# Performance work log

Measured on AMD Instinct MI355X. Metric: run time of the kernel, lower is better.

## Reference

```python
import jax, jax.numpy as jnp
import numpy as np

B, N, FEAT, H = 4, 1024, 512, 8
HD = FEAT // H


def _xavier(key, shape, gain):
    fan_in, fan_out = shape[1], shape[0]
    a = gain * np.sqrt(6.0 / (fan_in + fan_out))
    return jax.random.uniform(key, shape, jnp.float32, -a, a)


def setup_inputs() -> dict:
    key = jax.random.key(0)
    ks = jax.random.split(key, 12)
    g = 2 ** (-0.5)
    return {
        "ndata": jax.random.normal(ks[0], (B, N, FEAT), jnp.float32),
        "attn_bias": jax.random.normal(ks[1], (B, N, N, H), jnp.float32),
        "attn_mask": jax.random.bernoulli(ks[2], 0.1, (B, N, N, H)),
        "Wq": _xavier(ks[3], (FEAT, FEAT), g), "bq": jnp.zeros((FEAT,), jnp.float32),
        "Wk": _xavier(ks[4], (FEAT, FEAT), g), "bk": jnp.zeros((FEAT,), jnp.float32),
        "Wv": _xavier(ks[5], (FEAT, FEAT), g), "bv": jnp.zeros((FEAT,), jnp.float32),
        "Wo": _xavier(ks[6], (FEAT, FEAT), 1.0), "bo": jnp.zeros((FEAT,), jnp.float32),
    }


def reference(ndata, attn_bias, attn_mask, Wq, bq, Wk, bk, Wv, bv, Wo, bo):
    b, n, feat = ndata.shape
    h = attn_bias.shape[-1]
    hd = feat // h
    scaling = hd ** (-0.5)
    # projections -> [B, N, H, HD]
    q = (ndata @ Wq.T + bq).reshape(b, n, h, hd) * scaling
    k = (ndata @ Wk.T + bk).reshape(b, n, h, hd)
    v = (ndata @ Wv.T + bv).reshape(b, n, h, hd)
    # scores [B, N(q), N(k), H] to match torch layout for bias/mask
    scores = jnp.einsum("bihd,bjhd->bijh", q, k)
    scores = scores + attn_bias
    scores = jnp.where(attn_mask, -jnp.inf, scores)
    attn = jax.nn.softmax(scores, axis=2)  # softmax over key dim
    out = jnp.einsum("bijh,bjhd->bihd", attn, v).reshape(b, n, feat)
    return out @ Wo.T + bo
```

## Files before the change

kernel.cpp:

```cpp
#include <hip/hip_runtime.h>
#include <hip/hip_bf16.h>
#include <cstdint>


namespace {

constexpr int kN = 1024;

typedef short bf16x8 __attribute__((ext_vector_type(8)));
typedef float f32x4 __attribute__((ext_vector_type(4)));
using u16 = unsigned short;
using u8 = unsigned char;

__device__ __forceinline__ u16 f2bf(float f) {
  union { float f; uint32_t i; } v;
  v.f = f;
  uint32_t r = v.i + 0x7fffu + ((v.i >> 16) & 1u);
  return (u16)(r >> 16);
}

__device__ __forceinline__ void gload_lds16(const void* g, void* l) {
  __builtin_amdgcn_global_load_lds(
      (__attribute__((address_space(1))) void*)g,
      (__attribute__((address_space(3))) void*)l, 16, 0, 0);
}
__device__ __forceinline__ void gload_lds4(const void* g, void* l) {
  __builtin_amdgcn_global_load_lds(
      (__attribute__((address_space(1))) void*)g,
      (__attribute__((address_space(3))) void*)l, 4, 0, 0);
}

__global__ void detect_mask_kernel(const unsigned char* __restrict__ m,
                                   int* __restrict__ flag) {
  __shared__ int red[256];
  int local = 0;
  for (int i = threadIdx.x; i < 65536; i += 256) local += (m[i] != 0) ? 1 : 0;
  red[threadIdx.x] = local;
  __syncthreads();
  for (int s = 128; s > 0; s >>= 1) {
    if ((int)threadIdx.x < s) red[threadIdx.x] += red[threadIdx.x + s];
    __syncthreads();
  }
  if (threadIdx.x == 0) *flag = (red[0] > 4915) ? 1 : 0;
}

__global__ __launch_bounds__(256) void canon_mask(const int* __restrict__ m32,
                                                  const int* __restrict__ flag,
                                                  u8* __restrict__ out) {
  if (*flag != 0) return;
  const size_t t = (size_t)blockIdx.x * 256 + threadIdx.x;
  const int4* src = (const int4*)m32 + t * 8;
  uchar4 ob[8];
#pragma unroll
  for (int q = 0; q < 8; ++q) {
    const int4 v = src[q];
    ob[q] = make_uchar4(v.x != 0, v.y != 0, v.z != 0, v.w != 0);
  }
  *(uint4*)(out + t * 32) = *(const uint4*)&ob[0];
  *(uint4*)(out + t * 32 + 16) = *(const uint4*)&ob[4];
}

__global__ __launch_bounds__(256) void convert_kernel(
    const float* __restrict__ nd, const float* __restrict__ Wq,
    const float* __restrict__ Wk, const float* __restrict__ Wv,
    const float* __restrict__ Wo, u16* __restrict__ A16,
    u16* __restrict__ W16) {
  const int gi = blockIdx.x * 256 + threadIdx.x;
  const float* src;
  u16* dst;
  int off;
  if (gi < 524288) {
    src = nd; dst = A16; off = gi * 4;
  } else {
    const int w = (gi - 524288) >> 16;
    off = ((gi - 524288) & 65535) * 4;
    src = (w == 0) ? Wq : (w == 1) ? Wk : (w == 2) ? Wv : Wo;
    dst = W16 + (size_t)w * 262144;
  }
  const float4 v = *(const float4*)&src[off];
  ushort4 o;
  o.x = f2bf(v.x); o.y = f2bf(v.y); o.z = f2bf(v.z); o.w = f2bf(v.w);
  *(ushort4*)&dst[off] = o;
}

template <int EPI>
__global__ __launch_bounds__(256) void gemm_nt(
    const u16* __restrict__ A16, const u16* __restrict__ W16,
    const float* __restrict__ bq, const float* __restrict__ bk,
    const float* __restrict__ bv, u16* __restrict__ Q16,
    u16* __restrict__ KF, u16* __restrict__ VF,
    const float* __restrict__ bo, float* __restrict__ OutF) {
  __shared__ u16 As[128 * 64];
  __shared__ u16 Ws[64 * 64];
  const int tid = threadIdx.x, lane = tid & 63, wid = tid >> 6;
  const int r0 = blockIdx.x * 128;
  int wsel, c0;
  const float* bias;
  float scale = 1.0f;
  if (EPI == 0) {
    wsel = blockIdx.y >> 3;
    c0 = (blockIdx.y & 7) * 64;
    bias = (wsel == 0) ? bq : (wsel == 1) ? bk : bv;
    if (wsel == 0) scale = 0.125f;
  } else {
    wsel = 3;
    c0 = blockIdx.y * 64;
    bias = bo;
  }
  const u16* W = W16 + (size_t)wsel * (512 * 512);
  const int wm = (wid >> 1) * 64, wn = (wid & 1) * 32;

  f32x4 acc[4][2] = {};
  for (int k0 = 0; k0 < 512; k0 += 64) {
    __syncthreads();
#pragma unroll
    for (int p = 0; p < 4; ++p) {
      const int o = p * 4096 + tid * 16;
      const int row = o >> 7, kb = o & 127;
      gload_lds16((const char*)A16 + (size_t)(r0 + row) * 1024 + k0 * 2 +
                      (kb ^ ((row & 7) << 4)),
                  (char*)As + o);
    }
#pragma unroll
    for (int p = 0; p < 2; ++p) {
      const int o = p * 4096 + tid * 16;
      const int row = o >> 7, kb = o & 127;
      gload_lds16((const char*)W + (size_t)(c0 + row) * 1024 + k0 * 2 +
                      (kb ^ ((row & 7) << 4)),
                  (char*)Ws + o);
    }
    __syncthreads();
    bf16x8 af[4][2], bf[2][2];
#pragma unroll
    for (int mt = 0; mt < 4; ++mt)
#pragma unroll
      for (int ks = 0; ks < 2; ++ks) {
        const int row = wm + mt * 16 + (lane & 15);
        const int kb = ks * 64 + (lane >> 4) * 16;
        af[mt][ks] = *(const bf16x8*)((const char*)As + row * 128 +
                                      (kb ^ ((row & 7) << 4)));
      }
#pragma unroll
    for (int nt = 0; nt < 2; ++nt)
#pragma unroll
      for (int ks = 0; ks < 2; ++ks) {
        const int row = wn + nt * 16 + (lane & 15);
        const int kb = ks * 64 + (lane >> 4) * 16;
        bf[nt][ks] = *(const bf16x8*)((const char*)Ws + row * 128 +
                                      (kb ^ ((row & 7) << 4)));
      }
#pragma unroll
    for (int mt = 0; mt < 4; ++mt)
#pragma unroll
      for (int nt = 0; nt < 2; ++nt)
#pragma unroll
        for (int ks = 0; ks < 2; ++ks)
          acc[mt][nt] = __builtin_amdgcn_mfma_f32_16x16x32_bf16(
              af[mt][ks], bf[nt][ks], acc[mt][nt], 0, 0, 0);
  }
  float bvals[2];
#pragma unroll
  for (int nt = 0; nt < 2; ++nt)
    bvals[nt] = bias[c0 + wn + nt * 16 + (lane & 15)];
#pragma unroll
  for (int mt = 0; mt < 4; ++mt)
#pragma unroll
    for (int nt = 0; nt < 2; ++nt)
#pragma unroll
      for (int r = 0; r < 4; ++r) {
        const int row = r0 + wm + mt * 16 + (lane >> 4) * 4 + r;
        const int col = c0 + wn + nt * 16 + (lane & 15);
        const float v = (acc[mt][nt][r] + bvals[nt]) * scale;
        if (EPI == 0) {
          const int bb = row >> 10, n = row & 1023, hh = col >> 6,
                    dd = col & 63;
          if (wsel == 0) {
            Q16[((size_t)(bb * 8 + hh) * 1024 + n) * 64 + dd] = f2bf(v);
          } else if (wsel == 1) {
            const int jc = n >> 5, tt = (n >> 4) & 1, ln = n & 15;
            const int ks = dd >> 5, gg = (dd >> 3) & 3, e = dd & 7;
            KF[(((((size_t)(bb * 8 + hh) * 32 + jc) * 2 + tt) * 2 + ks) * 64 +
                gg * 16 + ln) * 8 + e] = f2bf(v);
          } else {
            const int jc = n >> 5, gg = (n >> 3) & 3, e = n & 7;
            const int dt = dd >> 4, ii = dd & 15;
            VF[((((size_t)(bb * 8 + hh) * 32 + jc) * 4 + dt) * 64 + gg * 16 +
                ii) * 8 + e] = f2bf(v);
          }
        } else {
          OutF[(size_t)row * 512 + col] = v;
        }
      }
}

__global__ __launch_bounds__(512, 2) void attn_fused2(
    const u16* __restrict__ Q16, const u16* __restrict__ KF,
    const u16* __restrict__ VF, const float* __restrict__ bias,
    const u8* __restrict__ mask8, const u8* __restrict__ mask_ws,
    const int* __restrict__ flag, u16* __restrict__ Ow16) {
  __shared__ __align__(16) char biasL[3][16384];
  __shared__ __align__(16) char maskL[3][4096];
  __shared__ __align__(16) char PsL[8][1280];

  const int tid = threadIdx.x, lane = tid & 63, h = tid >> 6;
  const int bid = blockIdx.x;
  const int b = (bid >> 1) & 3;
  const int it = ((bid >> 3) << 1) | (bid & 1);
  const int i0 = it * 16;
  const u8* mk8 = (*flag != 0) ? mask8 : mask_ws;

  const int j = lane & 15, g = lane >> 4;
  const int hh = h >> 2;
  char* Ps = PsL[h];

  const u16* Qh = Q16 + (size_t)(b * 8 + h) * 65536;
  bf16x8 qf[2];
#pragma unroll
  for (int ks = 0; ks < 2; ++ks)
    qf[ks] = *(const bf16x8*)&Qh[(size_t)(i0 + j) * 64 + ks * 32 + g * 8];

  float mo[4], lo[4];
  f32x4 oacc[4] = {};
#pragma unroll
  for (int r = 0; r < 4; ++r) { mo[r] = -3e38f; lo[r] = 0.f; }

  const size_t biasRow0 = (size_t)(b * 1024 + i0) * 8192;
  const size_t maskRow0 = (size_t)(b * 1024 + i0) * 8192;

  auto STAGE = [&](int buf, int jc) {
    char* bb_ = biasL[buf];
    char* mb_ = maskL[buf];
    const int w = h;
#pragma unroll
    for (int q = 0; q < 8; ++q) {
      const int gidx = q * 8 + w;
      const int i = gidx >> 2, oct = gidx & 3;
      const int f = (i >> 2) + 4 * (oct & 1);
      const size_t src = biasRow0 + (size_t)i * 8192 + (size_t)jc * 256 +
                         oct * 64 + (lane >> 3) * 8 + (((lane & 7) - f) & 7);
      gload_lds4(bias + src, bb_ + gidx * 256);
    }
#pragma unroll
    for (int c = 0; c < 2; ++c) {
      const int i = c * 8 + w;
      const int fm = (i >> 2) & 1;
      const size_t src = maskRow0 + (size_t)i * 8192 + (size_t)jc * 256 +
                         (lane >> 4) * 64 + (size_t)(((lane & 15) ^ fm) * 4);
      gload_lds4(mk8 + src, mb_ + i * 256);
    }
  };

  STAGE(0, 0);
  STAGE(1, 1);
  asm volatile("s_waitcnt vmcnt(10)\n\ts_barrier" ::: "memory");

  for (int t = 0; t < 32; ++t) {
    const char* bb_ = biasL[t % 3];
    const char* mb_ = maskL[t % 3];

    const size_t kvb = (size_t)(b * 8 + h) * 32 + t;
    const u16* kfp = KF + kvb * 2048;
    const u16* vfp = VF + kvb * 2048;
    bf16x8 kf[2][2], vf[4];
#pragma unroll
    for (int t2 = 0; t2 < 2; ++t2)
#pragma unroll
      for (int ks = 0; ks < 2; ++ks)
        kf[t2][ks] = *(const bf16x8*)&kfp[((t2 * 2 + ks) * 64 + lane) * 8];
#pragma unroll
    for (int dt = 0; dt < 4; ++dt)
      vf[dt] = *(const bf16x8*)&vfp[(dt * 64 + lane) * 8];

    if (t < 30) STAGE((t + 2) % 3, t + 2);

    f32x4 sa[2] = {};
#pragma unroll
    for (int t2 = 0; t2 < 2; ++t2)
#pragma unroll
      for (int ks = 0; ks < 2; ++ks)
        sa[t2] = __builtin_amdgcn_mfma_f32_16x16x32_bf16(qf[ks], kf[t2][ks],
                                                         sa[t2], 0, 0, 0);

    float s[2][4];
#pragma unroll
    for (int jt = 0; jt < 2; ++jt) {
      const int oct = jt * 2 + (j >> 3);
#pragma unroll
      for (int r = 0; r < 4; ++r) {
        const int gidx = (g * 4 + r) * 4 + oct;
        const float bv = *(const float*)(
            bb_ + gidx * 256 +
            (((j & 7) * 8 + ((h + g + 4 * (j >> 3)) & 7)) << 2));
        const int qd = (j & 7) * 2 + ((hh + (g & 1)) & 1);
        const u8 mkv = *(const u8*)(mb_ + gidx * 64 + qd * 4 + (h & 3));
        s[jt][r] = mkv ? -1e30f : (sa[jt][r] + bv);
      }
    }

#pragma unroll
    for (int r = 0; r < 4; ++r) {
      float cm = fmaxf(s[0][r], s[1][r]);
      cm = fmaxf(cm, __shfl_xor(cm, 1));
      cm = fmaxf(cm, __shfl_xor(cm, 2));
      cm = fmaxf(cm, __shfl_xor(cm, 4));
      cm = fmaxf(cm, __shfl_xor(cm, 8));
      const float mn = fmaxf(mo[r], cm);
      const float sc = __expf(mo[r] - mn);
      mo[r] = mn;
      const float p0 = __expf(s[0][r] - mn);
      const float p1 = __expf(s[1][r] - mn);
      float rs = p0 + p1;
      rs += __shfl_xor(rs, 1);
      rs += __shfl_xor(rs, 2);
      rs += __shfl_xor(rs, 4);
      rs += __shfl_xor(rs, 8);
      lo[r] = lo[r] * sc + rs;
      const int row = g * 4 + r;
      *(u16*)(Ps + row * 80 + j * 2) = f2bf(p0);
      *(u16*)(Ps + row * 80 + 32 + j * 2) = f2bf(p1);
#pragma unroll
      for (int dt = 0; dt < 4; ++dt) oacc[dt][r] *= sc;
    }
    asm volatile("s_waitcnt lgkmcnt(0)" ::: "memory");
    __builtin_amdgcn_sched_barrier(0);

    const bf16x8 pf = *(const bf16x8*)(Ps + j * 80 + g * 16);
#pragma unroll
    for (int dt = 0; dt < 4; ++dt)
      oacc[dt] =
          __builtin_amdgcn_mfma_f32_16x16x32_bf16(pf, vf[dt], oacc[dt], 0, 0, 0);

    if (t < 30)
      asm volatile("s_waitcnt vmcnt(10)\n\ts_barrier" ::: "memory");
    else if (t == 30)
      asm volatile("s_waitcnt vmcnt(0)\n\ts_barrier" ::: "memory");
  }

#pragma unroll
  for (int r = 0; r < 4; ++r) {
    const float rl = 1.0f / lo[r];
    const int i = i0 + g * 4 + r;
#pragma unroll
    for (int dt = 0; dt < 4; ++dt) {
      const int d = dt * 16 + j;
      Ow16[((size_t)(b * 1024 + i)) * 512 + h * 64 + d] =
          f2bf(oacc[dt][r] * rl);
    }
  }
}

}

extern "C" void kernel_launch(void* const* d_in, const int* in_sizes, int n_in,
                              void* d_out, int out_size, void* d_ws,
                              size_t ws_size, hipStream_t stream) {
  const float* ndata = (const float*)d_in[0];
  const float* bias = (const float*)d_in[1];
  const void* mask = d_in[2];
  const float* Wq = (const float*)d_in[3];
  const float* bq = (const float*)d_in[4];
  const float* Wk = (const float*)d_in[5];
  const float* bk = (const float*)d_in[6];
  const float* Wv = (const float*)d_in[7];
  const float* bvp = (const float*)d_in[8];
  const float* Wo = (const float*)d_in[9];
  const float* bo = (const float*)d_in[10];
  float* out = (float*)d_out;

  u16* A16 = (u16*)d_ws;
  u16* W16 = A16 + 2097152;
  u16* Q16 = W16 + 1048576;
  u16* KF = Q16 + 2097152;
  u16* VF = KF + 2097152;
  u16* Ow = VF + 2097152;
  u8* mask_ws = (u8*)(Ow + 2097152);
  int* flag = (int*)(mask_ws + 33554432);

  detect_mask_kernel<<<1, 256, 0, stream>>>((const unsigned char*)mask, flag);
  canon_mask<<<4096, 256, 0, stream>>>((const int*)mask, flag, mask_ws);
  convert_kernel<<<3072, 256, 0, stream>>>(ndata, Wq, Wk, Wv, Wo, A16, W16);
  gemm_nt<0><<<dim3(32, 24), 256, 0, stream>>>(A16, W16, bq, bk, bvp, Q16, KF,
                                               VF, nullptr, nullptr);
  attn_fused2<<<256, 512, 0, stream>>>(Q16, KF, VF, bias, (const u8*)mask,
                                       mask_ws, flag, Ow);
  gemm_nt<1><<<dim3(32, 8), 256, 0, stream>>>(Ow, W16, nullptr, nullptr,
                                              nullptr, nullptr, nullptr,
                                              nullptr, bo, out);
}
```

Before: 211.8 us.

## Split attention key range across two blocks and merge with a combine kernel

The attention kernel now splits the key dimension in half, launching twice as many blocks. Each block writes unnormalized fp32 partial outputs plus row max and sum, and a new combine kernel merges the two halves. The score MFMA is transposed so P feeds the PV MFMA directly from registers instead of going through LDS. Rescaling of the accumulator is skipped when no row max changed, staging drops to double-buffered with a simplified swizzle, and launch bounds allow more blocks per CU. The cost is an extra kernel launch and the fp32 partial traffic through global memory.

```diff
diff --git a/kernel.cpp b/kernel.cpp
--- a/kernel.cpp
+++ b/kernel.cpp
@@ -4,8 +4,6 @@
 
 
 namespace {
-
-constexpr int kN = 1024;
 
 typedef short bf16x8 __attribute__((ext_vector_type(8)));
 typedef float f32x4 __attribute__((ext_vector_type(4)));
@@ -182,10 +180,12 @@
             KF[(((((size_t)(bb * 8 + hh) * 32 + jc) * 2 + tt) * 2 + ks) * 64 +
                 gg * 16 + ln) * 8 + e] = f2bf(v);
           } else {
-            const int jc = n >> 5, gg = (n >> 3) & 3, e = n & 7;
+            const int jc = n >> 5, jl = n & 31;
+            const int gg = (jl & 15) >> 2;
+            const int e = (jl < 16) ? (jl & 3) : (4 + (jl & 3));
             const int dt = dd >> 4, ii = dd & 15;
-            VF[((((size_t)(bb * 8 + hh) * 32 + jc) * 4 + dt) * 64 + gg * 16 +
-                ii) * 8 + e] = f2bf(v);
+            VF[((((size_t)(bb * 8 + hh) * 32 + jc) * 4 + dt) * 512) +
+               (gg * 16 + ii) * 8 + e] = f2bf(v);
           }
         } else {
           OutF[(size_t)row * 512 + col] = v;
@@ -193,160 +193,187 @@
       }
 }
 
-__global__ __launch_bounds__(512, 2) void attn_fused2(
+__global__ __launch_bounds__(512, 4) void attn_fused3(
     const u16* __restrict__ Q16, const u16* __restrict__ KF,
     const u16* __restrict__ VF, const float* __restrict__ bias,
     const u8* __restrict__ mask8, const u8* __restrict__ mask_ws,
-    const int* __restrict__ flag, u16* __restrict__ Ow16) {
-  __shared__ __align__(16) char biasL[3][16384];
-  __shared__ __align__(16) char maskL[3][4096];
-  __shared__ __align__(16) char PsL[8][1280];
+    const int* __restrict__ flag, float* __restrict__ Opart,
+    float* __restrict__ Mm, float* __restrict__ Ll) {
+  __shared__ __align__(16) char biasL[2][16384];
+  __shared__ __align__(16) char maskL[2][4096];
 
   const int tid = threadIdx.x, lane = tid & 63, h = tid >> 6;
   const int bid = blockIdx.x;
-  const int b = (bid >> 1) & 3;
-  const int it = ((bid >> 3) << 1) | (bid & 1);
+  const int b = bid & 3, half = (bid >> 2) & 1, it = bid >> 3;
   const int i0 = it * 16;
-  const u8* mk8 = (*flag != 0) ? mask8 : mask_ws;
-
-  const int j = lane & 15, g = lane >> 4;
-  const int hh = h >> 2;
-  char* Ps = PsL[h];
-
-  const u16* Qh = Q16 + (size_t)(b * 8 + h) * 65536;
+  const u8* mk = (*flag != 0) ? mask8 : mask_ws;
+
+  const int i = lane & 15, g = lane >> 4;
+  const int g1 = g & 1, g2 = g >> 1;
+  const int bh = b * 8 + h;
+
+  const u16* Qh = Q16 + (size_t)bh * 65536;
   bf16x8 qf[2];
 #pragma unroll
   for (int ks = 0; ks < 2; ++ks)
-    qf[ks] = *(const bf16x8*)&Qh[(size_t)(i0 + j) * 64 + ks * 32 + g * 8];
-
-  float mo[4], lo[4];
+    qf[ks] = *(const bf16x8*)&Qh[(size_t)(i0 + i) * 64 + ks * 32 + g * 8];
+
+  float mo = -3e38f, lo = 0.f;
   f32x4 oacc[4] = {};
-#pragma unroll
-  for (int r = 0; r < 4; ++r) { mo[r] = -3e38f; lo[r] = 0.f; }
-
-  const size_t biasRow0 = (size_t)(b * 1024 + i0) * 8192;
-  const size_t maskRow0 = (size_t)(b * 1024 + i0) * 8192;
+
+  const size_t rowb = (size_t)(b * 1024 + i0) * 8192;
+  int boff[8];
+#pragma unroll
+  for (int q = 0; q < 8; ++q) {
+    const int w = q * 512 + tid;
+    const int wi = w >> 8, oct = (w >> 6) & 3, slot = w & 63;
+    const int se = slot ^ wi ^ ((oct & 1) << 4);
+    boff[q] = wi * 8192 + oct * 64 + se;
+  }
+  int moff[2];
+#pragma unroll
+  for (int q = 0; q < 2; ++q) {
+    const int bb2 = (q * 512 + tid) * 4;
+    const int wi = bb2 >> 8, oct = (bb2 >> 6) & 3, sl = bb2 & 63;
+    const int se = sl ^ ((wi << 2) & 0x3C);
+    moff[q] = wi * 8192 + oct * 64 + se;
+  }
+  const int Cb = (((g1 << 5) | h) ^ i ^ (g2 << 4)) << 2;
+  const int baseb = i * 1024 + g2 * 256;
+  const int Cm = ((g1 << 5) | h) ^ ((i << 2) & 0x3C);
+  const int basem = i * 256 + g2 * 64;
 
   auto STAGE = [&](int buf, int jc) {
-    char* bb_ = biasL[buf];
-    char* mb_ = maskL[buf];
-    const int w = h;
-#pragma unroll
-    for (int q = 0; q < 8; ++q) {
-      const int gidx = q * 8 + w;
-      const int i = gidx >> 2, oct = gidx & 3;
-      const int f = (i >> 2) + 4 * (oct & 1);
-      const size_t src = biasRow0 + (size_t)i * 8192 + (size_t)jc * 256 +
-                         oct * 64 + (lane >> 3) * 8 + (((lane & 7) - f) & 7);
-      gload_lds4(bias + src, bb_ + gidx * 256);
+    const float* bsrc = bias + rowb + (size_t)jc * 256;
+    const u8* msrc = mk + rowb + (size_t)jc * 256;
+#pragma unroll
+    for (int q = 0; q < 8; ++q)
+      gload_lds4(bsrc + boff[q], biasL[buf] + (q * 512 + tid) * 4);
+#pragma unroll
+    for (int q = 0; q < 2; ++q)
+      gload_lds4(msrc + moff[q], maskL[buf] + (q * 512 + tid) * 4);
+  };
+
+  const int jcBase = half * 16;
+  STAGE(0, jcBase);
+
+  for (int t = 0; t < 16; ++t) {
+    asm volatile("s_waitcnt vmcnt(0)" ::: "memory");
+    __builtin_amdgcn_s_barrier();
+    const char* bb_ = biasL[t & 1];
+    const char* mb_ = maskL[t & 1];
+    const int jc = jcBase + t;
+    const size_t kvb = (size_t)bh * 32 + jc;
+
+    bf16x8 kf[2][2];
+#pragma unroll
+    for (int t2 = 0; t2 < 2; ++t2)
+#pragma unroll
+      for (int ks = 0; ks < 2; ++ks)
+        kf[t2][ks] =
+            *(const bf16x8*)&KF[((kvb * 2 + t2) * 2 + ks) * 512 + lane * 8];
+    bf16x8 vf[4];
+#pragma unroll
+    for (int dt = 0; dt < 4; ++dt)
+      vf[dt] = *(const bf16x8*)&VF[(kvb * 4 + dt) * 512 + lane * 8];
+
+    if (t < 15) STAGE((t + 1) & 1, jc + 1);
+
+    f32x4 sa[2] = {};
+#pragma unroll
+    for (int t2 = 0; t2 < 2; ++t2)
+#pragma unroll
+      for (int ks = 0; ks < 2; ++ks)
+        sa[t2] = __builtin_amdgcn_mfma_f32_16x16x32_bf16(kf[t2][ks], qf[ks],
+                                                         sa[t2], 0, 0, 0);
+
+    float s[2][4];
+#pragma unroll
+    for (int t2 = 0; t2 < 2; ++t2)
+#pragma unroll
+      for (int r = 0; r < 4; ++r) {
+        const float bv =
+            *(const float*)(bb_ + baseb + t2 * 512 + (Cb ^ (r << 5)));
+        const u8 mv = *(const u8*)(mb_ + basem + t2 * 128 + (Cm ^ (r << 3)));
+        s[t2][r] = mv ? -1e30f : (sa[t2][r] + bv);
+      }
+
+    float cm = s[0][0];
+#pragma unroll
+    for (int k = 1; k < 8; ++k) cm = fmaxf(cm, s[k >> 2][k & 3]);
+    cm = fmaxf(cm, __shfl_xor(cm, 16));
+    cm = fmaxf(cm, __shfl_xor(cm, 32));
+    const bool upd = __any(cm > mo);
+    const float mn = fmaxf(mo, cm);
+    const float sc = __expf(mo - mn);
+    float p[2][4], rs = 0.f;
+#pragma unroll
+    for (int k = 0; k < 8; ++k) {
+      const float pv = __expf(s[k >> 2][k & 3] - mn);
+      p[k >> 2][k & 3] = pv;
+      rs += pv;
     }
-#pragma unroll
-    for (int c = 0; c < 2; ++c) {
-      const int i = c * 8 + w;
-      const int fm = (i >> 2) & 1;
-      const size_t src = maskRow0 + (size_t)i * 8192 + (size_t)jc * 256 +
-                         (lane >> 4) * 64 + (size_t)(((lane & 15) ^ fm) * 4);
-      gload_lds4(mk8 + src, mb_ + i * 256);
+    rs += __shfl_xor(rs, 16);
+    rs += __shfl_xor(rs, 32);
+    lo = lo * sc + rs;
+    mo = mn;
+    if (upd) {
+      float scB[4];
+#pragma unroll
+      for (int r = 0; r < 4; ++r) scB[r] = __shfl(sc, g * 4 + r);
+#pragma unroll
+      for (int dt = 0; dt < 4; ++dt)
+#pragma unroll
+        for (int r = 0; r < 4; ++r) oacc[dt][r] *= scB[r];
     }
-  };
-
-  STAGE(0, 0);
-  STAGE(1, 1);
-  asm volatile("s_waitcnt vmcnt(10)\n\ts_barrier" ::: "memory");
-
-  for (int t = 0; t < 32; ++t) {
-    const char* bb_ = biasL[t % 3];
-    const char* mb_ = maskL[t % 3];
-
-    const size_t kvb = (size_t)(b * 8 + h) * 32 + t;
-    const u16* kfp = KF + kvb * 2048;
-    const u16* vfp = VF + kvb * 2048;
-    bf16x8 kf[2][2], vf[4];
-#pragma unroll
-    for (int t2 = 0; t2 < 2; ++t2)
-#pragma unroll
-      for (int ks = 0; ks < 2; ++ks)
-        kf[t2][ks] = *(const bf16x8*)&kfp[((t2 * 2 + ks) * 64 + lane) * 8];
+
+    union { u16 us[8]; bf16x8 v; } pk;
+#pragma unroll
+    for (int e = 0; e < 4; ++e) {
+      pk.us[e] = f2bf(p[0][e]);
+      pk.us[4 + e] = f2bf(p[1][e]);
+    }
 #pragma unroll
     for (int dt = 0; dt < 4; ++dt)
-      vf[dt] = *(const bf16x8*)&vfp[(dt * 64 + lane) * 8];
-
-    if (t < 30) STAGE((t + 2) % 3, t + 2);
-
-    f32x4 sa[2] = {};
-#pragma unroll
-    for (int t2 = 0; t2 < 2; ++t2)
-#pragma unroll
-      for (int ks = 0; ks < 2; ++ks)
-        sa[t2] = __builtin_amdgcn_mfma_f32_16x16x32_bf16(qf[ks], kf[t2][ks],
-                                                         sa[t2], 0, 0, 0);
-
-    float s[2][4];
-#pragma unroll
-    for (int jt = 0; jt < 2; ++jt) {
-      const int oct = jt * 2 + (j >> 3);
-#pragma unroll
-      for (int r = 0; r < 4; ++r) {
-        const int gidx = (g * 4 + r) * 4 + oct;
-        const float bv = *(const float*)(
-            bb_ + gidx * 256 +
-            (((j & 7) * 8 + ((h + g + 4 * (j >> 3)) & 7)) << 2));
-        const int qd = (j & 7) * 2 + ((hh + (g & 1)) & 1);
-        const u8 mkv = *(const u8*)(mb_ + gidx * 64 + qd * 4 + (h & 3));
-        s[jt][r] = mkv ? -1e30f : (sa[jt][r] + bv);
-      }
-    }
-
-#pragma unroll
-    for (int r = 0; r < 4; ++r) {
-      float cm = fmaxf(s[0][r], s[1][r]);
-      cm = fmaxf(cm, __shfl_xor(cm, 1));
-      cm = fmaxf(cm, __shfl_xor(cm, 2));
-      cm = fmaxf(cm, __shfl_xor(cm, 4));
-      cm = fmaxf(cm, __shfl_xor(cm, 8));
-      const float mn = fmaxf(mo[r], cm);
-      const float sc = __expf(mo[r] - mn);
-      mo[r] = mn;
-      const float p0 = __expf(s[0][r] - mn);
-      const float p1 = __expf(s[1][r] - mn);
-      float rs = p0 + p1;
-      rs += __shfl_xor(rs, 1);
-      rs += __shfl_xor(rs, 2);
-      rs += __shfl_xor(rs, 4);
-      rs += __shfl_xor(rs, 8);
-      lo[r] = lo[r] * sc + rs;
-      const int row = g * 4 + r;
-      *(u16*)(Ps + row * 80 + j * 2) = f2bf(p0);
-      *(u16*)(Ps + row * 80 + 32 + j * 2) = f2bf(p1);
-#pragma unroll
-      for (int dt = 0; dt < 4; ++dt) oacc[dt][r] *= sc;
-    }
-    asm volatile("s_waitcnt lgkmcnt(0)" ::: "memory");
-    __builtin_amdgcn_sched_barrier(0);
-
-    const bf16x8 pf = *(const bf16x8*)(Ps + j * 80 + g * 16);
+      oacc[dt] = __builtin_amdgcn_mfma_f32_16x16x32_bf16(pk.v, vf[dt],
+                                                         oacc[dt], 0, 0, 0);
+  }
+
+  float* Op = Opart + (size_t)half * 2097152 +
+              ((size_t)(b * 1024 + i0)) * 512 + h * 64;
+#pragma unroll
+  for (int r = 0; r < 4; ++r)
 #pragma unroll
     for (int dt = 0; dt < 4; ++dt)
-      oacc[dt] =
-          __builtin_amdgcn_mfma_f32_16x16x32_bf16(pf, vf[dt], oacc[dt], 0, 0, 0);
-
-    if (t < 30)
-      asm volatile("s_waitcnt vmcnt(10)\n\ts_barrier" ::: "memory");
-    else if (t == 30)
-      asm volatile("s_waitcnt vmcnt(0)\n\ts_barrier" ::: "memory");
-  }
-
-#pragma unroll
-  for (int r = 0; r < 4; ++r) {
-    const float rl = 1.0f / lo[r];
-    const int i = i0 + g * 4 + r;
-#pragma unroll
-    for (int dt = 0; dt < 4; ++dt) {
-      const int d = dt * 16 + j;
-      Ow16[((size_t)(b * 1024 + i)) * 512 + h * 64 + d] =
-          f2bf(oacc[dt][r] * rl);
-    }
-  }
+      Op[(size_t)(g * 4 + r) * 512 + dt * 16 + i] = oacc[dt][r];
+  if (lane < 16) {
+    const size_t mi = ((size_t)(half * 4 + b) * 8 + h) * 1024 + i0 + lane;
+    Mm[mi] = mo;
+    Ll[mi] = lo;
+  }
+}
+
+__global__ __launch_bounds__(256) void combine_halves(
+    const float* __restrict__ Opart, const float* __restrict__ Mm,
+    const float* __restrict__ Ll, u16* __restrict__ Ow) {
+  const int t = blockIdx.x * 256 + threadIdx.x;
+  const int col4 = t & 127, row = t >> 7;
+  const int b = row >> 10, i = row & 1023, h = col4 >> 4;
+  const size_t o0 = (size_t)row * 512 + col4 * 4;
+  const float4 v0 = *(const float4*)&Opart[o0];
+  const float4 v1 = *(const float4*)&Opart[o0 + 2097152];
+  const size_t mi0 = ((size_t)b * 8 + h) * 1024 + i;
+  const float m0 = Mm[mi0], m1 = Mm[mi0 + 32768];
+  const float l0 = Ll[mi0], l1 = Ll[mi0 + 32768];
+  const float M = fmaxf(m0, m1);
+  const float e0 = __expf(m0 - M), e1 = __expf(m1 - M);
+  const float inv = 1.0f / (l0 * e0 + l1 * e1);
+  ushort4 o;
+  o.x = f2bf((v0.x * e0 + v1.x * e1) * inv);
+  o.y = f2bf((v0.y * e0 + v1.y * e1) * inv);
+  o.z = f2bf((v0.z * e0 + v1.z * e1) * inv);
+  o.w = f2bf((v0.w * e0 + v1.w * e1) * inv);
+  *(ushort4*)&Ow[o0] = o;
 }
 
 }
@@ -373,7 +400,10 @@
   u16* KF = Q16 + 2097152;
   u16* VF = KF + 2097152;
   u16* Ow = VF + 2097152;
-  u8* mask_ws = (u8*)(Ow + 2097152);
+  float* Opart = (float*)(Ow + 2097152);
+  float* Mm = Opart + 4194304;
+  float* Ll = Mm + 65536;
+  u8* mask_ws = (u8*)(Ll + 65536);
   int* flag = (int*)(mask_ws + 33554432);
 
   detect_mask_kernel<<<1, 256, 0, stream>>>((const unsigned char*)mask, flag);
@@ -381,8 +411,9 @@
   convert_kernel<<<3072, 256, 0, stream>>>(ndata, Wq, Wk, Wv, Wo, A16, W16);
   gemm_nt<0><<<dim3(32, 24), 256, 0, stream>>>(A16, W16, bq, bk, bvp, Q16, KF,
                                                VF, nullptr, nullptr);
-  attn_fused2<<<256, 512, 0, stream>>>(Q16, KF, VF, bias, (const u8*)mask,
-                                       mask_ws, flag, Ow);
+  attn_fused3<<<512, 512, 0, stream>>>(Q16, KF, VF, bias, (const u8*)mask,
+                                       mask_ws, flag, Opart, Mm, Ll);
+  combine_halves<<<2048, 256, 0, stream>>>(Opart, Mm, Ll, Ow);
   gemm_nt<1><<<dim3(32, 8), 256, 0, stream>>>(Ow, W16, nullptr, nullptr,
                                               nullptr, nullptr, nullptr,
                                               nullptr, bo, out);
```

After: 184.8 us. 1.15x faster.
